# Kernel tuning notes

Measured on AMD Instinct MI355X. Metric: run time of the kernel, lower is better.

Reference implementation:

```python
import jax, jax.numpy as jnp
import numpy as np

N_NODES = 50000
N_EDGES = 800000
IN_CH = 64
HID_CH = 128


def setup_inputs() -> dict:
    key = jax.random.key(0)
    k1, k2, k3 = jax.random.split(key, 3)
    x = jax.random.normal(k1, (N_NODES, IN_CH), dtype=jnp.float32)
    edge_index = jax.random.randint(k2, (2, N_EDGES), 0, N_NODES, dtype=jnp.int64)
    # lin_l weight of SAGEConv: [hidden_channels, in_channels]
    W = jax.random.normal(k3, (HID_CH, IN_CH), dtype=jnp.float32) * (1.0 / np.sqrt(IN_CH))
    return {"x": x, "edge_index": edge_index, "W": W}


def reference(x, edge_index, W):
    src = edge_index[0]  # message sources
    dst = edge_index[1]  # aggregation targets
    msgs = x[src]  # [E, in] gather
    summed = jax.ops.segment_sum(msgs, dst, num_segments=N_NODES)  # [N, in]
    counts = jax.ops.segment_sum(jnp.ones((msgs.shape[0],), dtype=x.dtype), dst,
                                 num_segments=N_NODES)  # [N]
    mean = summed / jnp.maximum(counts, 1.0)[:, None]  # mean aggregation (0 for isolated nodes)
    # lin_l: no bias, no root_weight -> out = mean @ W^T
    return jnp.einsum('ni,oi->no', mean, W)
```

## Files before the change

kernel.cpp:

```cpp
#include <hip/hip_runtime.h>


constexpr int N_NODES = 50000;
constexpr int N_EDGES = 800000;
constexpr int IN_CH   = 64;
constexpr int HID_CH  = 128;

constexpr int NBKT          = 256;
constexpr int NODES_PER_BKT = 196;
constexpr int BKT_CAP       = 4096;
constexpr int CHUNK         = 4096;
constexpr int NBIN          = (N_EDGES + CHUNK - 1) / CHUNK;

__global__ __launch_bounds__(256) void bin_kernel(
    const int* __restrict__ ei,
    int* __restrict__ cursor,
    unsigned long long* __restrict__ binned)
{
    __shared__ int hist[NBKT];
    __shared__ int scan[NBKT];
    __shared__ int lexcl[NBKT];
    __shared__ int lcur[NBKT];
    __shared__ int res[NBKT];
    __shared__ unsigned long long stage[CHUNK];

    const int t  = threadIdx.x;
    const int e0 = blockIdx.x * CHUNK;
    const int nE = min(N_EDGES - e0, CHUNK);

    hist[t] = 0;
    __syncthreads();

    int srcs[16], dsts[16];
    #pragma unroll
    for (int q = 0; q < 4; ++q) {
        const int idx = t * 16 + q * 4;
        if (idx < nE) {
            const int4 s4 = *reinterpret_cast<const int4*>(ei + e0 + idx);
            const int4 d4 = *reinterpret_cast<const int4*>(ei + N_EDGES + e0 + idx);
            srcs[q * 4 + 0] = s4.x; srcs[q * 4 + 1] = s4.y;
            srcs[q * 4 + 2] = s4.z; srcs[q * 4 + 3] = s4.w;
            dsts[q * 4 + 0] = d4.x; dsts[q * 4 + 1] = d4.y;
            dsts[q * 4 + 2] = d4.z; dsts[q * 4 + 3] = d4.w;
            atomicAdd(&hist[d4.x / NODES_PER_BKT], 1);
            atomicAdd(&hist[d4.y / NODES_PER_BKT], 1);
            atomicAdd(&hist[d4.z / NODES_PER_BKT], 1);
            atomicAdd(&hist[d4.w / NODES_PER_BKT], 1);
        } else {
            srcs[q*4+0]=srcs[q*4+1]=srcs[q*4+2]=srcs[q*4+3]=0;
            dsts[q*4+0]=dsts[q*4+1]=dsts[q*4+2]=dsts[q*4+3]=0;
        }
    }
    __syncthreads();

    const int hv = hist[t];
    scan[t] = hv;
    __syncthreads();
    for (int off = 1; off < NBKT; off <<= 1) {
        const int u = (t >= off) ? scan[t - off] : 0;
        __syncthreads();
        scan[t] += u;
        __syncthreads();
    }
    const int myExcl = scan[t] - hv;
    lexcl[t] = myExcl;
    lcur[t]  = myExcl;
    res[t]   = (hv > 0) ? atomicAdd(&cursor[t], hv) : 0;
    __syncthreads();

    #pragma unroll
    for (int q = 0; q < 16; ++q) {
        const int idx = t * 16 + q;
        if (idx < nE) {
            const int b = dsts[q] / NODES_PER_BKT;
            const int p = atomicAdd(&lcur[b], 1);
            stage[p] = ((unsigned long long)(unsigned)dsts[q] << 32) | (unsigned)srcs[q];
        }
    }
    __syncthreads();

    for (int i = t; i < nE; i += 256) {
        const unsigned long long v = stage[i];
        const int b = (int)(v >> 32) / NODES_PER_BKT;
        const int p = res[b] + (i - lexcl[b]);
        if (p < BKT_CAP) binned[(size_t)b * BKT_CAP + p] = v;
    }
}

__global__ __launch_bounds__(256) void csr_build_kernel(
    const unsigned long long* __restrict__ binned,
    const int* __restrict__ cursor,
    int* __restrict__ offs,
    int* __restrict__ csr_src)
{
    __shared__ int bsum[NBKT];
    __shared__ int ldeg[NODES_PER_BKT];
    __shared__ int lscan[NBKT];
    __shared__ int lcur[NODES_PER_BKT];
    __shared__ int stage_src[BKT_CAP];

    const int b = blockIdx.x;
    const int t = threadIdx.x;

    const int cAll = min(cursor[t], BKT_CAP);
    bsum[t] = cAll;
    if (t < NODES_PER_BKT) ldeg[t] = 0;
    __syncthreads();
    for (int off = 1; off < NBKT; off <<= 1) {
        const int u = (t >= off) ? bsum[t - off] : 0;
        __syncthreads();
        bsum[t] += u;
        __syncthreads();
    }
    const int cnt   = min(cursor[b], BKT_CAP);
    const int ebase = bsum[b] - cnt;
    const int nodeBase = b * NODES_PER_BKT;

    unsigned long long ev[16];
    #pragma unroll
    for (int q = 0; q < 16; ++q) {
        const int i = t + q * 256;
        ev[q] = 0;
        if (i < cnt) {
            ev[q] = binned[(size_t)b * BKT_CAP + i];
            atomicAdd(&ldeg[(int)(ev[q] >> 32) - nodeBase], 1);
        }
    }
    __syncthreads();

    const int dv = (t < NODES_PER_BKT) ? ldeg[t] : 0;
    lscan[t] = dv;
    __syncthreads();
    for (int off = 1; off < NBKT; off <<= 1) {
        const int u = (t >= off) ? lscan[t - off] : 0;
        __syncthreads();
        lscan[t] += u;
        __syncthreads();
    }
    const int nNodes = min(N_NODES - nodeBase, NODES_PER_BKT);
    if (t < nNodes) {
        const int excl = lscan[t] - dv;
        offs[nodeBase + t] = ebase + excl;
        lcur[t] = excl;
    }
    if (b == NBKT - 1 && t == 0) offs[N_NODES] = N_EDGES;
    __syncthreads();

    #pragma unroll
    for (int q = 0; q < 16; ++q) {
        const int i = t + q * 256;
        if (i < cnt) {
            const int loc = (int)(ev[q] >> 32) - nodeBase;
            const int p = atomicAdd(&lcur[loc], 1);
            stage_src[p] = (int)(ev[q] & 0xffffffffu);
        }
    }
    __syncthreads();

    for (int i = t; i < cnt; i += 256) {
        csr_src[ebase + i] = stage_src[i];
    }
}

__global__ __launch_bounds__(256) void gather_fused_kernel(
    const float* __restrict__ x,
    const int*   __restrict__ csr_src,
    const int*   __restrict__ offs,
    const float* __restrict__ W,
    float*       __restrict__ out)
{
    __shared__ float4 sW4[16][HID_CH + 1];
    __shared__ float4 sM[4][16];

    const int t = threadIdx.x;
    #pragma unroll
    for (int r = 0; r < 8; ++r) {
        const int i = t + r * 256;
        const int o = i >> 4, k4 = i & 15;
        sW4[k4][o] = *reinterpret_cast<const float4*>(W + (size_t)o * IN_CH + k4 * 4);
    }
    __syncthreads();

    const int wave = t >> 6;
    const int lane = t & 63;
    const int grp  = lane >> 4;
    const int ch4  = lane & 15;
    const int wid  = blockIdx.x * 4 + wave;

    #pragma unroll 1
    for (int j = 0; j < 4; ++j) {
        const int n = wid * 4 + j;
        const int start = offs[n];
        const int end   = offs[n + 1];
        const int d     = end - start;

        float a0 = 0.f, a1 = 0.f, a2 = 0.f, a3 = 0.f;
        for (int base = start; base < end; base += 64) {
            const int cnt = min(end - base, 64);
            int idx = 0;
            if (lane < cnt) idx = csr_src[base + lane];
            const int nIt = (cnt + 3) >> 2;
            for (int i = 0; i < nIt; i += 4) {
                const int e0 = 4 * i + grp;
                const int e1 = e0 + 4, e2 = e0 + 8, e3 = e0 + 12;
                const int s0 = __shfl(idx, e0 & 63, 64);
                const int s1 = __shfl(idx, e1 & 63, 64);
                const int s2 = __shfl(idx, e2 & 63, 64);
                const int s3 = __shfl(idx, e3 & 63, 64);
                const float f0 = (e0 < cnt) ? 1.f : 0.f;
                const float f1 = (e1 < cnt) ? 1.f : 0.f;
                const float f2 = (e2 < cnt) ? 1.f : 0.f;
                const float f3 = (e3 < cnt) ? 1.f : 0.f;
                const float4 v0 = *reinterpret_cast<const float4*>(x + (size_t)s0 * IN_CH + ch4 * 4);
                const float4 v1 = *reinterpret_cast<const float4*>(x + (size_t)s1 * IN_CH + ch4 * 4);
                const float4 v2 = *reinterpret_cast<const float4*>(x + (size_t)s2 * IN_CH + ch4 * 4);
                const float4 v3 = *reinterpret_cast<const float4*>(x + (size_t)s3 * IN_CH + ch4 * 4);
                a0 = fmaf(f0, v0.x, a0); a1 = fmaf(f0, v0.y, a1);
                a2 = fmaf(f0, v0.z, a2); a3 = fmaf(f0, v0.w, a3);
                a0 = fmaf(f1, v1.x, a0); a1 = fmaf(f1, v1.y, a1);
                a2 = fmaf(f1, v1.z, a2); a3 = fmaf(f1, v1.w, a3);
                a0 = fmaf(f2, v2.x, a0); a1 = fmaf(f2, v2.y, a1);
                a2 = fmaf(f2, v2.z, a2); a3 = fmaf(f2, v2.w, a3);
                a0 = fmaf(f3, v3.x, a0); a1 = fmaf(f3, v3.y, a1);
                a2 = fmaf(f3, v3.z, a2); a3 = fmaf(f3, v3.w, a3);
            }
        }
        #pragma unroll
        for (int m = 16; m <= 32; m <<= 1) {
            a0 += __shfl_xor(a0, m, 64);
            a1 += __shfl_xor(a1, m, 64);
            a2 += __shfl_xor(a2, m, 64);
            a3 += __shfl_xor(a3, m, 64);
        }
        const float inv = 1.0f / fmaxf((float)d, 1.0f);
        if (lane < 16) {
            float4 r{a0 * inv, a1 * inv, a2 * inv, a3 * inv};
            sM[wave][ch4] = r;
        }
        __asm__ volatile("s_waitcnt lgkmcnt(0)" ::: "memory");
        __builtin_amdgcn_sched_barrier(0);

        float o0 = 0.f, o1 = 0.f;
        #pragma unroll
        for (int k4 = 0; k4 < 16; ++k4) {
            const float4 w0 = sW4[k4][lane];
            const float4 w1 = sW4[k4][lane + 64];
            const float4 a  = sM[wave][k4];
            o0 += a.x * w0.x + a.y * w0.y + a.z * w0.z + a.w * w0.w;
            o1 += a.x * w1.x + a.y * w1.y + a.z * w1.z + a.w * w1.w;
        }
        const size_t row = (size_t)n * HID_CH;
        out[row + lane]      = o0;
        out[row + 64 + lane] = o1;
    }
}

extern "C" void kernel_launch(void* const* d_in, const int* in_sizes, int n_in,
                              void* d_out, int out_size, void* d_ws, size_t ws_size,
                              hipStream_t stream) {
    const float* x   = (const float*)d_in[0];
    const int*   ei  = (const int*)  d_in[1];
    const float* W   = (const float*)d_in[2];
    float*       out = (float*)d_out;

    unsigned long long* binned = (unsigned long long*)d_ws;
    int* cursor  = (int*)(binned + (size_t)NBKT * BKT_CAP);
    int* offs    = cursor + NBKT;
    int* csr_src = offs + 50004;

    hipMemsetAsync(cursor, 0, NBKT * sizeof(int), stream);
    bin_kernel<<<NBIN, 256, 0, stream>>>(ei, cursor, binned);
    csr_build_kernel<<<NBKT, 256, 0, stream>>>(binned, cursor, offs, csr_src);
    gather_fused_kernel<<<N_NODES / 16, 256, 0, stream>>>(x, csr_src, offs, W, out);
}
```

Before: 141.8 us.

## Pack edge bins to 32 bits, use wave-shuffle scans, batch per-wave gather

Edge bins now store dst and src packed into one 32-bit word (16 bits each, which fits node ids below 65536) instead of 64 bits. This halves the staging and global traffic in the bin and CSR-build kernels. The shared-memory Hillis-Steele scans are replaced by wave-level shuffle scans plus a small cross-wave fixup, which cuts barrier count. The gather kernel moves to 512-thread blocks and loads all four nodes' offsets and first index chunks up front so more loads are in flight. It then does one batched projection for four nodes per wave, at the cost of higher register use and a hard 16-bit limit on node ids.

```diff
diff --git a/kernel.cpp b/kernel.cpp
--- a/kernel.cpp
+++ b/kernel.cpp
@@ -15,18 +15,20 @@
 __global__ __launch_bounds__(256) void bin_kernel(
     const int* __restrict__ ei,
     int* __restrict__ cursor,
-    unsigned long long* __restrict__ binned)
+    unsigned* __restrict__ binned)
 {
     __shared__ int hist[NBKT];
-    __shared__ int scan[NBKT];
     __shared__ int lexcl[NBKT];
     __shared__ int lcur[NBKT];
     __shared__ int res[NBKT];
-    __shared__ unsigned long long stage[CHUNK];
-
-    const int t  = threadIdx.x;
-    const int e0 = blockIdx.x * CHUNK;
-    const int nE = min(N_EDGES - e0, CHUNK);
+    __shared__ int wsum[4];
+    __shared__ unsigned stage[CHUNK];
+
+    const int t    = threadIdx.x;
+    const int wave = t >> 6;
+    const int lane = t & 63;
+    const int e0   = blockIdx.x * CHUNK;
+    const int nE   = min(N_EDGES - e0, CHUNK);
 
     hist[t] = 0;
     __syncthreads();
@@ -54,15 +56,18 @@
     __syncthreads();
 
     const int hv = hist[t];
-    scan[t] = hv;
-    __syncthreads();
-    for (int off = 1; off < NBKT; off <<= 1) {
-        const int u = (t >= off) ? scan[t - off] : 0;
-        __syncthreads();
-        scan[t] += u;
-        __syncthreads();
-    }
-    const int myExcl = scan[t] - hv;
+    int v = hv;
+    #pragma unroll
+    for (int off = 1; off < 64; off <<= 1) {
+        const int u = __shfl_up(v, off, 64);
+        if (lane >= off) v += u;
+    }
+    if (lane == 63) wsum[wave] = v;
+    __syncthreads();
+    int prefix = 0;
+    #pragma unroll
+    for (int k = 0; k < 4; ++k) prefix += (k < wave) ? wsum[k] : 0;
+    const int myExcl = v + prefix - hv;
     lexcl[t] = myExcl;
     lcur[t]  = myExcl;
     res[t]   = (hv > 0) ? atomicAdd(&cursor[t], hv) : 0;
@@ -74,72 +79,74 @@
         if (idx < nE) {
             const int b = dsts[q] / NODES_PER_BKT;
             const int p = atomicAdd(&lcur[b], 1);
-            stage[p] = ((unsigned long long)(unsigned)dsts[q] << 32) | (unsigned)srcs[q];
+            stage[p] = ((unsigned)dsts[q] << 16) | (unsigned)srcs[q];
         }
     }
     __syncthreads();
 
     for (int i = t; i < nE; i += 256) {
-        const unsigned long long v = stage[i];
-        const int b = (int)(v >> 32) / NODES_PER_BKT;
+        const unsigned pv = stage[i];
+        const int b = (int)(pv >> 16) / NODES_PER_BKT;
         const int p = res[b] + (i - lexcl[b]);
-        if (p < BKT_CAP) binned[(size_t)b * BKT_CAP + p] = v;
+        if (p < BKT_CAP) binned[(size_t)b * BKT_CAP + p] = pv;
     }
 }
 
 __global__ __launch_bounds__(256) void csr_build_kernel(
-    const unsigned long long* __restrict__ binned,
+    const unsigned* __restrict__ binned,
     const int* __restrict__ cursor,
     int* __restrict__ offs,
     int* __restrict__ csr_src)
 {
-    __shared__ int bsum[NBKT];
     __shared__ int ldeg[NODES_PER_BKT];
-    __shared__ int lscan[NBKT];
     __shared__ int lcur[NODES_PER_BKT];
+    __shared__ int wsum[4];
     __shared__ int stage_src[BKT_CAP];
 
-    const int b = blockIdx.x;
-    const int t = threadIdx.x;
-
-    const int cAll = min(cursor[t], BKT_CAP);
-    bsum[t] = cAll;
+    const int b    = blockIdx.x;
+    const int t    = threadIdx.x;
+    const int wave = t >> 6;
+    const int lane = t & 63;
+
+    int contrib = (t < b) ? min(cursor[t], BKT_CAP) : 0;
+    #pragma unroll
+    for (int m = 1; m <= 32; m <<= 1) contrib += __shfl_xor(contrib, m, 64);
+    if (lane == 0) wsum[wave] = contrib;
     if (t < NODES_PER_BKT) ldeg[t] = 0;
     __syncthreads();
-    for (int off = 1; off < NBKT; off <<= 1) {
-        const int u = (t >= off) ? bsum[t - off] : 0;
-        __syncthreads();
-        bsum[t] += u;
-        __syncthreads();
-    }
-    const int cnt   = min(cursor[b], BKT_CAP);
-    const int ebase = bsum[b] - cnt;
+    const int ebase = wsum[0] + wsum[1] + wsum[2] + wsum[3];
+
+    const int cnt      = min(cursor[b], BKT_CAP);
     const int nodeBase = b * NODES_PER_BKT;
 
-    unsigned long long ev[16];
+    unsigned pk[16];
     #pragma unroll
     for (int q = 0; q < 16; ++q) {
         const int i = t + q * 256;
-        ev[q] = 0;
+        pk[q] = 0xffffffffu;
         if (i < cnt) {
-            ev[q] = binned[(size_t)b * BKT_CAP + i];
-            atomicAdd(&ldeg[(int)(ev[q] >> 32) - nodeBase], 1);
+            pk[q] = binned[(size_t)b * BKT_CAP + i];
+            atomicAdd(&ldeg[(int)(pk[q] >> 16) - nodeBase], 1);
         }
     }
     __syncthreads();
 
     const int dv = (t < NODES_PER_BKT) ? ldeg[t] : 0;
-    lscan[t] = dv;
-    __syncthreads();
-    for (int off = 1; off < NBKT; off <<= 1) {
-        const int u = (t >= off) ? lscan[t - off] : 0;
-        __syncthreads();
-        lscan[t] += u;
-        __syncthreads();
-    }
+    int v = dv;
+    #pragma unroll
+    for (int off = 1; off < 64; off <<= 1) {
+        const int u = __shfl_up(v, off, 64);
+        if (lane >= off) v += u;
+    }
+    if (lane == 63) wsum[wave] = v;
+    __syncthreads();
+    int prefix = 0;
+    #pragma unroll
+    for (int k = 0; k < 4; ++k) prefix += (k < wave) ? wsum[k] : 0;
+    const int excl = v + prefix - dv;
+
     const int nNodes = min(N_NODES - nodeBase, NODES_PER_BKT);
     if (t < nNodes) {
-        const int excl = lscan[t] - dv;
         offs[nodeBase + t] = ebase + excl;
         lcur[t] = excl;
     }
@@ -150,9 +157,9 @@
     for (int q = 0; q < 16; ++q) {
         const int i = t + q * 256;
         if (i < cnt) {
-            const int loc = (int)(ev[q] >> 32) - nodeBase;
+            const int loc = (int)(pk[q] >> 16) - nodeBase;
             const int p = atomicAdd(&lcur[loc], 1);
-            stage_src[p] = (int)(ev[q] & 0xffffffffu);
+            stage_src[p] = (int)(pk[q] & 0xffffu);
         }
     }
     __syncthreads();
@@ -162,20 +169,20 @@
     }
 }
 
-__global__ __launch_bounds__(256) void gather_fused_kernel(
+__global__ __launch_bounds__(512, 6) void gather_fused_kernel(
     const float* __restrict__ x,
     const int*   __restrict__ csr_src,
     const int*   __restrict__ offs,
     const float* __restrict__ W,
     float*       __restrict__ out)
 {
-    __shared__ float4 sW4[16][HID_CH + 1];
-    __shared__ float4 sM[4][16];
+    __shared__ float4 sW4[16][HID_CH];
+    __shared__ float4 sM[8][4][16];
 
     const int t = threadIdx.x;
     #pragma unroll
-    for (int r = 0; r < 8; ++r) {
-        const int i = t + r * 256;
+    for (int r = 0; r < 4; ++r) {
+        const int i = t + r * 512;
         const int o = i >> 4, k4 = i & 15;
         sW4[k4][o] = *reinterpret_cast<const float4*>(W + (size_t)o * IN_CH + k4 * 4);
     }
@@ -185,73 +192,101 @@
     const int lane = t & 63;
     const int grp  = lane >> 4;
     const int ch4  = lane & 15;
-    const int wid  = blockIdx.x * 4 + wave;
-
-    #pragma unroll 1
+    const int wid  = blockIdx.x * 8 + wave;
+    const int n0   = wid * 4;
+    if (n0 >= N_NODES) return;
+
+    int ov = 0;
+    if (lane < 5) ov = offs[min(n0 + lane, N_NODES)];
+    const int s0 = __shfl(ov, 0, 64), s1 = __shfl(ov, 1, 64);
+    const int s2 = __shfl(ov, 2, 64), s3 = __shfl(ov, 3, 64);
+    const int s4 = __shfl(ov, 4, 64);
+
+    int idxA = 0, idxB = 0, idxC = 0, idxD = 0;
+    if (lane < s1 - s0) idxA = csr_src[s0 + lane];
+    if (lane < s2 - s1) idxB = csr_src[s1 + lane];
+    if (lane < s3 - s2) idxC = csr_src[s2 + lane];
+    if (lane < s4 - s3) idxD = csr_src[s3 + lane];
+
+#define GATHER_NODE(JJ, S, E, IDX0)                                                   \
+    {                                                                                 \
+        float a0 = 0.f, a1 = 0.f, a2 = 0.f, a3 = 0.f;                                 \
+        int idxr = IDX0;                                                              \
+        for (int base = (S); base < (E); base += 64) {                                \
+            const int cnt = min((E) - base, 64);                                      \
+            if (base != (S)) {                                                        \
+                idxr = 0;                                                             \
+                if (lane < cnt) idxr = csr_src[base + lane];                          \
+            }                                                                         \
+            const int nIt = (cnt + 15) >> 4;                                          \
+            for (int ii = 0; ii < nIt; ++ii) {                                        \
+                const int eb = ii * 16;                                               \
+                const int e0 = eb + grp, e1 = e0 + 4, e2 = e0 + 8, e3 = e0 + 12;      \
+                const int q0 = __shfl(idxr, e0 & 63, 64);                             \
+                const int q1 = __shfl(idxr, e1 & 63, 64);                             \
+                const int q2 = __shfl(idxr, e2 & 63, 64);                             \
+                const int q3 = __shfl(idxr, e3 & 63, 64);                             \
+                const float f0 = (e0 < cnt) ? 1.f : 0.f;                              \
+                const float f1 = (e1 < cnt) ? 1.f : 0.f;                              \
+                const float f2 = (e2 < cnt) ? 1.f : 0.f;                              \
+                const float f3 = (e3 < cnt) ? 1.f : 0.f;                              \
+                const float4 v0 = *reinterpret_cast<const float4*>(x + (size_t)q0 * IN_CH + ch4 * 4); \
+                const float4 v1 = *reinterpret_cast<const float4*>(x + (size_t)q1 * IN_CH + ch4 * 4); \
+                const float4 v2 = *reinterpret_cast<const float4*>(x + (size_t)q2 * IN_CH + ch4 * 4); \
+                const float4 v3 = *reinterpret_cast<const float4*>(x + (size_t)q3 * IN_CH + ch4 * 4); \
+                a0 = fmaf(f0, v0.x, a0); a1 = fmaf(f0, v0.y, a1);                     \
+                a2 = fmaf(f0, v0.z, a2); a3 = fmaf(f0, v0.w, a3);                     \
+                a0 = fmaf(f1, v1.x, a0); a1 = fmaf(f1, v1.y, a1);                     \
+                a2 = fmaf(f1, v1.z, a2); a3 = fmaf(f1, v1.w, a3);                     \
+                a0 = fmaf(f2, v2.x, a0); a1 = fmaf(f2, v2.y, a1);                     \
+                a2 = fmaf(f2, v2.z, a2); a3 = fmaf(f2, v2.w, a3);                     \
+                a0 = fmaf(f3, v3.x, a0); a1 = fmaf(f3, v3.y, a1);                     \
+                a2 = fmaf(f3, v3.z, a2); a3 = fmaf(f3, v3.w, a3);                     \
+            }                                                                         \
+        }                                                                             \
+        _Pragma("unroll")                                                             \
+        for (int m = 16; m <= 32; m <<= 1) {                                          \
+            a0 += __shfl_xor(a0, m, 64);                                              \
+            a1 += __shfl_xor(a1, m, 64);                                              \
+            a2 += __shfl_xor(a2, m, 64);                                              \
+            a3 += __shfl_xor(a3, m, 64);                                              \
+        }                                                                             \
+        if (lane < 16) {                                                              \
+            const float inv = 1.0f / fmaxf((float)((E) - (S)), 1.0f);                 \
+            float4 r{a0 * inv, a1 * inv, a2 * inv, a3 * inv};                         \
+            sM[wave][JJ][ch4] = r;                                                    \
+        }                                                                             \
+    }
+
+    GATHER_NODE(0, s0, s1, idxA)
+    GATHER_NODE(1, s1, s2, idxB)
+    GATHER_NODE(2, s2, s3, idxC)
+    GATHER_NODE(3, s3, s4, idxD)
+#undef GATHER_NODE
+
+    __asm__ volatile("s_waitcnt lgkmcnt(0)" ::: "memory");
+    __builtin_amdgcn_sched_barrier(0);
+
+    float acc[4][2] = {{0.f,0.f},{0.f,0.f},{0.f,0.f},{0.f,0.f}};
+    #pragma unroll
+    for (int k4 = 0; k4 < 16; ++k4) {
+        const float4 w0 = sW4[k4][lane];
+        const float4 w1 = sW4[k4][lane + 64];
+        #pragma unroll
+        for (int j = 0; j < 4; ++j) {
+            const float4 a = sM[wave][j][k4];
+            acc[j][0] += a.x * w0.x + a.y * w0.y + a.z * w0.z + a.w * w0.w;
+            acc[j][1] += a.x * w1.x + a.y * w1.y + a.z * w1.z + a.w * w1.w;
+        }
+    }
+    #pragma unroll
     for (int j = 0; j < 4; ++j) {
-        const int n = wid * 4 + j;
-        const int start = offs[n];
-        const int end   = offs[n + 1];
-        const int d     = end - start;
-
-        float a0 = 0.f, a1 = 0.f, a2 = 0.f, a3 = 0.f;
-        for (int base = start; base < end; base += 64) {
-            const int cnt = min(end - base, 64);
-            int idx = 0;
-            if (lane < cnt) idx = csr_src[base + lane];
-            const int nIt = (cnt + 3) >> 2;
-            for (int i = 0; i < nIt; i += 4) {
-                const int e0 = 4 * i + grp;
-                const int e1 = e0 + 4, e2 = e0 + 8, e3 = e0 + 12;
-                const int s0 = __shfl(idx, e0 & 63, 64);
-                const int s1 = __shfl(idx, e1 & 63, 64);
-                const int s2 = __shfl(idx, e2 & 63, 64);
-                const int s3 = __shfl(idx, e3 & 63, 64);
-                const float f0 = (e0 < cnt) ? 1.f : 0.f;
-                const float f1 = (e1 < cnt) ? 1.f : 0.f;
-                const float f2 = (e2 < cnt) ? 1.f : 0.f;
-                const float f3 = (e3 < cnt) ? 1.f : 0.f;
-                const float4 v0 = *reinterpret_cast<const float4*>(x + (size_t)s0 * IN_CH + ch4 * 4);
-                const float4 v1 = *reinterpret_cast<const float4*>(x + (size_t)s1 * IN_CH + ch4 * 4);
-                const float4 v2 = *reinterpret_cast<const float4*>(x + (size_t)s2 * IN_CH + ch4 * 4);
-                const float4 v3 = *reinterpret_cast<const float4*>(x + (size_t)s3 * IN_CH + ch4 * 4);
-                a0 = fmaf(f0, v0.x, a0); a1 = fmaf(f0, v0.y, a1);
-                a2 = fmaf(f0, v0.z, a2); a3 = fmaf(f0, v0.w, a3);
-                a0 = fmaf(f1, v1.x, a0); a1 = fmaf(f1, v1.y, a1);
-                a2 = fmaf(f1, v1.z, a2); a3 = fmaf(f1, v1.w, a3);
-                a0 = fmaf(f2, v2.x, a0); a1 = fmaf(f2, v2.y, a1);
-                a2 = fmaf(f2, v2.z, a2); a3 = fmaf(f2, v2.w, a3);
-                a0 = fmaf(f3, v3.x, a0); a1 = fmaf(f3, v3.y, a1);
-                a2 = fmaf(f3, v3.z, a2); a3 = fmaf(f3, v3.w, a3);
-            }
-        }
-        #pragma unroll
-        for (int m = 16; m <= 32; m <<= 1) {
-            a0 += __shfl_xor(a0, m, 64);
-            a1 += __shfl_xor(a1, m, 64);
-            a2 += __shfl_xor(a2, m, 64);
-            a3 += __shfl_xor(a3, m, 64);
-        }
-        const float inv = 1.0f / fmaxf((float)d, 1.0f);
-        if (lane < 16) {
-            float4 r{a0 * inv, a1 * inv, a2 * inv, a3 * inv};
-            sM[wave][ch4] = r;
-        }
-        __asm__ volatile("s_waitcnt lgkmcnt(0)" ::: "memory");
-        __builtin_amdgcn_sched_barrier(0);
-
-        float o0 = 0.f, o1 = 0.f;
-        #pragma unroll
-        for (int k4 = 0; k4 < 16; ++k4) {
-            const float4 w0 = sW4[k4][lane];
-            const float4 w1 = sW4[k4][lane + 64];
-            const float4 a  = sM[wave][k4];
-            o0 += a.x * w0.x + a.y * w0.y + a.z * w0.z + a.w * w0.w;
-            o1 += a.x * w1.x + a.y * w1.y + a.z * w1.z + a.w * w1.w;
-        }
-        const size_t row = (size_t)n * HID_CH;
-        out[row + lane]      = o0;
-        out[row + 64 + lane] = o1;
+        const int n = n0 + j;
+        if (n < N_NODES) {
+            const size_t row = (size_t)n * HID_CH;
+            out[row + lane]      = acc[j][0];
+            out[row + 64 + lane] = acc[j][1];
+        }
     }
 }
 
@@ -263,7 +298,7 @@
     const float* W   = (const float*)d_in[2];
     float*       out = (float*)d_out;
 
-    unsigned long long* binned = (unsigned long long*)d_ws;
+    unsigned* binned = (unsigned*)d_ws;
     int* cursor  = (int*)(binned + (size_t)NBKT * BKT_CAP);
     int* offs    = cursor + NBKT;
     int* csr_src = offs + 50004;
@@ -271,5 +306,5 @@
     hipMemsetAsync(cursor, 0, NBKT * sizeof(int), stream);
     bin_kernel<<<NBIN, 256, 0, stream>>>(ei, cursor, binned);
     csr_build_kernel<<<NBKT, 256, 0, stream>>>(binned, cursor, offs, csr_src);
-    gather_fused_kernel<<<N_NODES / 16, 256, 0, stream>>>(x, csr_src, offs, W, out);
+    gather_fused_kernel<<<(N_NODES + 31) / 32, 512, 0, stream>>>(x, csr_src, offs, W, out);
 }
```

New measurement: 557.8 us. 293% more time.
